# Kernel optimization log

Measured on AMD Instinct MI355X. Metric: run time of the kernel, lower is better.

## Reference

```python
import jax, jax.numpy as jnp
import numpy as np

B = 512       # batch
D = 256       # n_embd
NH = 4        # heads
NN = 8 * D // NH   # neurons per head = 512
NTOT = NH * NN     # 2048
DH = D // NH       # 64
K = 8              # thinking steps
EPS_LN = 1e-5


def _ln(x, g, b):
    mu = jnp.mean(x, axis=-1, keepdims=True)
    var = jnp.mean((x - mu) ** 2, axis=-1, keepdims=True)
    return (x - mu) * jax.lax.rsqrt(var + EPS_LN) * g + b


def setup_inputs() -> dict:
    key = jax.random.key(0)
    ks = jax.random.split(key, 12)
    s = 0.02
    w = lambda k, shape: (jax.random.normal(k, shape, jnp.float32) * s)
    return {
        "boards": jax.random.normal(ks[0], (B, 12, 8, 8), jnp.float32),
        # board_encoder: Linear(768,d) -> GELU -> LN(d) -> Linear(d,d); weights stored (in,out)
        "enc_w1": w(ks[1], (768, D)), "enc_b1": jnp.zeros((D,), jnp.float32),
        "enc_ln_g": jnp.ones((D,), jnp.float32), "enc_ln_b": jnp.zeros((D,), jnp.float32),
        "enc_w2": w(ks[2], (D, D)), "enc_b2": jnp.zeros((D,), jnp.float32),
        "xinit_w": w(ks[3], (D, NTOT)), "xinit_b": jnp.zeros((NTOT,), jnp.float32),
        "D_y": w(ks[4], (NH, D, NN)),
        "E": w(ks[5], (NTOT, D)),
        "D_x": w(ks[6], (NH, D, NN)),
        "By_w": w(ks[7], (D, D)),
        "Bx_w": w(ks[8], (D, D)),
        "lna_g": jnp.ones((D,), jnp.float32), "lna_b": jnp.zeros((D,), jnp.float32),
        "lnz_g": jnp.ones((D,), jnp.float32), "lnz_b": jnp.zeros((D,), jnp.float32),
        "log_damping": jnp.asarray(np.log(0.9 / 0.1), jnp.float32),
        "vh_w1": w(ks[9], (D, D // 2)), "vh_b1": jnp.zeros((D // 2,), jnp.float32),
        "vh_w2": w(ks[10], (D // 2, 1)), "vh_b2": jnp.zeros((1,), jnp.float32),
    }


def reference(boards, enc_w1, enc_b1, enc_ln_g, enc_ln_b, enc_w2, enc_b2,
              xinit_w, xinit_b, D_y, E, D_x, By_w, Bx_w,
              lna_g, lna_b, lnz_g, lnz_b, log_damping,
              vh_w1, vh_b1, vh_w2, vh_b2):
    Bn = boards.shape[0]
    flat = boards.reshape(Bn, 768)
    h = jax.nn.gelu(flat @ enc_w1 + enc_b1, approximate=False)
    h = _ln(h, enc_ln_g, enc_ln_b)
    b = h @ enc_w2 + enc_b2                      # (B, d)
    x0 = jax.nn.relu(b @ xinit_w + xinit_b)      # (B, n)
    rho0 = jnp.zeros((Bn, NH, NN, DH), boards.dtype)
    lam = jax.nn.sigmoid(log_damping)
    b_y = b @ By_w
    b_x = b @ Bx_w

    def step(carry, _):
        x, rho = carry
        x_h = x.reshape(Bn, NH, NN)
        a = jnp.einsum('bhnd,bhn->bhd', rho, x_h).reshape(Bn, D)   # read from scratchpad
        a_cond = _ln(a + b_y, lna_g, lna_b)
        g = jax.nn.relu(jnp.einsum('bd,hdn->bhn', a_cond, D_y))
        y = (g * x_h).reshape(Bn, NTOT)
        z = _ln(y @ E, lnz_g, lnz_b)
        dx = jax.nn.relu(jnp.einsum('bd,hdn->bhn', z + b_x, D_x))
        x_new = x + dx.reshape(Bn, NTOT)
        xh = x_new.reshape(Bn, NH, NN)
        x_write = xh / (jnp.linalg.norm(xh, axis=-1, keepdims=True) + 1e-8)
        z_h = z.reshape(Bn, NH, DH)
        rho_new = lam * rho + (1.0 - lam) * jnp.einsum('bhn,bhd->bhnd', x_write, z_h)
        return (x_new, rho_new), z

    (_, _), zs = jax.lax.scan(step, (x0, rho0), None, length=K)
    z_last = zs[-1]                              # (B, d) from final thinking step
    v = jnp.tanh(jax.nn.gelu(z_last @ vh_w1 + vh_b1, approximate=False) @ vh_w2 + vh_b2)
    return v                                     # (B, 1)
```

## Files before the change

kernel.cpp:

```cpp
#include <hip/hip_runtime.h>
#include <hip/hip_bf16.h>
#include <math.h>

#define B_ 512
#define D_ 256
#define NH_ 4
#define NN_ 512
#define NTOT_ 2048
#define DH_ 64
#define KSTEPS 8

typedef __attribute__((ext_vector_type(8))) short bf16x8;
typedef __attribute__((ext_vector_type(4))) float f32x4;

__device__ __forceinline__ float gelu_exact(float x) {
  return 0.5f * x * (1.0f + erff(x * 0.70710678118654752f));
}

__device__ __forceinline__ unsigned short f2b(float f) {
  union { float f; unsigned int u; } x; x.f = f;
  unsigned int u = x.u;
  unsigned int r = (u + 0x7FFFu + ((u >> 16) & 1u)) >> 16;
  return (unsigned short)r;
}

__device__ __forceinline__ float blockReduceSum256(float v, float* red) {
  int t = threadIdx.x;
  red[t] = v; __syncthreads();
  #pragma unroll
  for (int st = 128; st > 0; st >>= 1) {
    if (t < st) red[t] += red[t + st];
    __syncthreads();
  }
  float r = red[0];
  __syncthreads();
  return r;
}

template<int EPI>
__global__ __launch_bounds__(256) void gemm_mfma(
    const unsigned short* __restrict__ A, const unsigned short* __restrict__ W,
    const float* __restrict__ bias, const float* __restrict__ mul,
    const float* __restrict__ addto, float* __restrict__ outf,
    unsigned short* __restrict__ outb, int K, int N, int kchunk)
{
  __shared__ __align__(16) unsigned short As[64 * 64];
  __shared__ __align__(16) unsigned short Ws[64 * 64];
  const int t = threadIdx.x;
  const int lane = t & 63;
  const int w = t >> 6;
  const int wr = (w >> 1) * 32, wc = (w & 1) * 32;
  const int row0 = blockIdx.y * 64, col0 = blockIdx.x * 64;
  const int k0 = blockIdx.z * kchunk;

  f32x4 acc[2][2];
  #pragma unroll
  for (int i = 0; i < 2; i++)
    #pragma unroll
    for (int j = 0; j < 2; j++)
      acc[i][j] = (f32x4){0.f, 0.f, 0.f, 0.f};

  const int ar = t >> 3;
  const int ac = t & 7;

  for (int kt = 0; kt < kchunk; kt += 64) {
    const int kk = k0 + kt;
    #pragma unroll
    for (int p = 0; p < 2; p++) {
      int row = p * 32 + ar;
      int cs = ac ^ (row & 7);
      bf16x8 va = *(const bf16x8*)&A[(size_t)(row0 + row) * K + kk + cs * 8];
      *(bf16x8*)&As[row * 64 + ac * 8] = va;
      bf16x8 vb = *(const bf16x8*)&W[(size_t)(col0 + row) * K + kk + cs * 8];
      *(bf16x8*)&Ws[row * 64 + ac * 8] = vb;
    }
    __syncthreads();
    #pragma unroll
    for (int ks = 0; ks < 64; ks += 32) {
      bf16x8 af[2], bfr[2];
      #pragma unroll
      for (int i = 0; i < 2; i++) {
        int r = wr + i * 16 + (lane & 15);
        int cb = (ks + (lane >> 4) * 8) * 2;
        cb ^= (r & 7) << 4;
        af[i] = *(const bf16x8*)((const char*)As + r * 128 + cb);
      }
      #pragma unroll
      for (int j = 0; j < 2; j++) {
        int c = wc + j * 16 + (lane & 15);
        int cb = (ks + (lane >> 4) * 8) * 2;
        cb ^= (c & 7) << 4;
        bfr[j] = *(const bf16x8*)((const char*)Ws + c * 128 + cb);
      }
      #pragma unroll
      for (int i = 0; i < 2; i++)
        #pragma unroll
        for (int j = 0; j < 2; j++)
          acc[i][j] = __builtin_amdgcn_mfma_f32_16x16x32_bf16(af[i], bfr[j], acc[i][j], 0, 0, 0);
    }
    __syncthreads();
  }

  const int cr = (lane >> 4) * 4;
  const int cc = lane & 15;
  #pragma unroll
  for (int i = 0; i < 2; i++) {
    #pragma unroll
    for (int j = 0; j < 2; j++) {
      #pragma unroll
      for (int q = 0; q < 4; q++) {
        int r = row0 + wr + i * 16 + cr + q;
        int c = col0 + wc + j * 16 + cc;
        float v = acc[i][j][q];
        if (EPI == 0) {
          v += bias[c]; v = fmaxf(v, 0.f);
          outf[(size_t)r * N + c] = v;
        } else if (EPI == 1) {
          v = fmaxf(v, 0.f) * mul[(size_t)r * N + c];
          outb[(size_t)r * N + c] = f2b(v);
        } else if (EPI == 2) {
          outf[(size_t)blockIdx.z * (512 * (size_t)N) + (size_t)r * N + c] = v;
        } else {
          v = fmaxf(v, 0.f) + addto[(size_t)r * N + c];
          outf[(size_t)r * N + c] = v;
        }
      }
    }
  }
}

template<int ACT>
__global__ __launch_bounds__(256) void gemm_tile(
    const float* __restrict__ A, const float* __restrict__ W,
    const float* __restrict__ bias, float* __restrict__ out,
    int M, int N, int K, int kchunk)
{
  __shared__ float As[16][68];
  __shared__ float Bs[16][68];
  const int tid = threadIdx.x;
  const int row0 = blockIdx.y * 64;
  const int col0 = blockIdx.x * 64;
  const int k0 = blockIdx.z * kchunk;
  const int ty = tid >> 4, tx = tid & 15;
  const int ar = tid >> 4, ak = tid & 15;
  const int br = tid >> 6, bc = tid & 63;
  float acc[4][4] = {};
  for (int kk = k0; kk < k0 + kchunk; kk += 16) {
    #pragma unroll
    for (int i = 0; i < 4; i++) {
      int r = ar + i * 16;
      As[ak][r] = A[(size_t)(row0 + r) * K + kk + ak];
    }
    #pragma unroll
    for (int i = 0; i < 4; i++) {
      int kr = br + i * 4;
      Bs[kr][bc] = W[(size_t)(kk + kr) * N + col0 + bc];
    }
    __syncthreads();
    #pragma unroll
    for (int q = 0; q < 16; q++) {
      float4 av = *(const float4*)&As[q][ty * 4];
      float4 bv = *(const float4*)&Bs[q][tx * 4];
      float aa[4] = {av.x, av.y, av.z, av.w};
      float bb[4] = {bv.x, bv.y, bv.z, bv.w};
      #pragma unroll
      for (int i = 0; i < 4; i++)
        #pragma unroll
        for (int j = 0; j < 4; j++)
          acc[i][j] = fmaf(aa[i], bb[j], acc[i][j]);
    }
    __syncthreads();
  }
  const bool parts = (gridDim.z > 1);
  float* o = out + (parts ? (size_t)blockIdx.z * (size_t)M * N : (size_t)0);
  #pragma unroll
  for (int i = 0; i < 4; i++) {
    int r = row0 + ty * 4 + i;
    #pragma unroll
    for (int j = 0; j < 4; j++) {
      int c = col0 + tx * 4 + j;
      float v = acc[i][j];
      if (!parts) {
        if (bias) v += bias[c];
        if (ACT == 1) v = v > 0.f ? v : 0.f;
        else if (ACT == 2) v = gelu_exact(v);
      }
      o[(size_t)r * N + c] = v;
    }
  }
}

template<bool HEAD>
__global__ __launch_bounds__(256) void k_transpose_cvt(
    const float* __restrict__ in, unsigned short* __restrict__ out,
    int Kdim, int Ndim)
{
  __shared__ float T[64][65];
  const int n0 = blockIdx.x * 64, k0 = blockIdx.y * 64;
  const int tx = threadIdx.x & 63, ty = threadIdx.x >> 6;
  #pragma unroll
  for (int i = 0; i < 16; i++) {
    int k = k0 + ty + i * 4;
    int n = n0 + tx;
    float v;
    if (HEAD) v = in[((size_t)(n >> 9) * 256 + k) * 512 + (n & 511)];
    else      v = in[(size_t)k * Ndim + n];
    T[ty + i * 4][tx] = v;
  }
  __syncthreads();
  #pragma unroll
  for (int i = 0; i < 16; i++) {
    int n = n0 + ty + i * 4;
    out[(size_t)n * Kdim + k0 + tx] = f2b(T[tx][ty + i * 4]);
  }
}

__global__ __launch_bounds__(256) void k_cvt(
    const float* __restrict__ in, unsigned short* __restrict__ out, int n4)
{
  int i = blockIdx.x * 256 + threadIdx.x;
  if (i < n4) {
    float4 v = ((const float4*)in)[i];
    unsigned int u0 = (unsigned int)f2b(v.x) | ((unsigned int)f2b(v.y) << 16);
    unsigned int u1 = (unsigned int)f2b(v.z) | ((unsigned int)f2b(v.w) << 16);
    ((uint2*)out)[i] = make_uint2(u0, u1);
  }
}

__global__ __launch_bounds__(256) void k_ln_reduce(
    const float* __restrict__ in, int nparts, int stride,
    const float* __restrict__ pre_bias, int do_gelu,
    const float* __restrict__ g, const float* __restrict__ bta,
    const float* __restrict__ addvec, float* __restrict__ out,
    unsigned short* __restrict__ out2_bf)
{
  __shared__ float red[256];
  int b = blockIdx.x, d = threadIdx.x;
  float v = 0.f;
  for (int p = 0; p < nparts; p++) v += in[(size_t)p * stride + (size_t)b * 256 + d];
  if (pre_bias) v += pre_bias[d];
  if (do_gelu) v = gelu_exact(v);
  float mu = blockReduceSum256(v, red) * (1.f / 256.f);
  float c = v - mu;
  float var = blockReduceSum256(c * c, red) * (1.f / 256.f);
  float vn = c * rsqrtf(var + 1e-5f) * g[d] + bta[d];
  out[(size_t)b * 256 + d] = vn;
  if (out2_bf) out2_bf[(size_t)b * 256 + d] = f2b(vn + addvec[(size_t)b * 256 + d]);
}

__global__ __launch_bounds__(256) void step_a(
    const float* __restrict__ x, float* __restrict__ xw_hist,
    const float* __restrict__ z_hist, const float* __restrict__ b_y,
    const float* __restrict__ lna_g, const float* __restrict__ lna_b,
    const float* __restrict__ log_damp, int k, unsigned short* __restrict__ out)
{
  __shared__ float dots[KSTEPS][NH_];
  __shared__ float red[256];
  int b = blockIdx.x, t = threadIdx.x;
  int lane = t & 63, wv = t >> 6;
  float lam = 1.f / (1.f + expf(-log_damp[0]));
  const float* xb = x + (size_t)b * NTOT_;
  float xv[8];
  #pragma unroll
  for (int i = 0; i < 8; i++) xv[i] = xb[t * 8 + i];

  if (k >= 1) {
    float s = 0.f;
    #pragma unroll
    for (int i = 0; i < 8; i++) s += xv[i] * xv[i];
    #pragma unroll
    for (int m = 1; m < 64; m <<= 1) s += __shfl_xor(s, m, 64);
    float inv = 1.f / (sqrtf(s) + 1e-8f);
    float* xwout = xw_hist + ((size_t)(k - 1) * B_ + b) * NTOT_;
    #pragma unroll
    for (int i = 0; i < 8; i++) xwout[t * 8 + i] = xv[i] * inv;
    if (lane == 0) dots[k - 1][wv] = s * inv;
  }
  for (int j = 0; j < k - 1; j++) {
    const float* xwb = xw_hist + ((size_t)j * B_ + b) * NTOT_;
    float s = 0.f;
    #pragma unroll
    for (int i = 0; i < 8; i++) s += xv[i] * xwb[t * 8 + i];
    #pragma unroll
    for (int off = 32; off > 0; off >>= 1) s += __shfl_down(s, off, 64);
    if (lane == 0) dots[j][wv] = s;
  }
  __syncthreads();

  int d = t;
  float av = 0.f, lp = 1.f;
  for (int j = k - 1; j >= 0; j--) {
    av += (1.f - lam) * lp * dots[j][d >> 6] * z_hist[((size_t)j * B_ + b) * D_ + d];
    lp *= lam;
  }
  av += b_y[(size_t)b * D_ + d];
  float mu = blockReduceSum256(av, red) * (1.f / 256.f);
  float c = av - mu;
  float var = blockReduceSum256(c * c, red) * (1.f / 256.f);
  out[(size_t)b * D_ + d] = f2b(c * rsqrtf(var + 1e-5f) * lna_g[d] + lna_b[d]);
}

__global__ __launch_bounds__(128) void k_value2(
    const float* __restrict__ gbuf, const float* __restrict__ w2,
    const float* __restrict__ b2, float* __restrict__ out)
{
  int b = blockIdx.x * blockDim.x + threadIdx.x;
  float s = 0.f;
  #pragma unroll 8
  for (int i = 0; i < 128; i++) s += gbuf[(size_t)b * 128 + i] * w2[i];
  out[b] = tanhf(s + b2[0]);
}

extern "C" void kernel_launch(void* const* d_in, const int* in_sizes, int n_in,
                              void* d_out, int out_size, void* d_ws, size_t ws_size,
                              hipStream_t stream) {
  const float* boards   = (const float*)d_in[0];
  const float* enc_w1   = (const float*)d_in[1];
  const float* enc_b1   = (const float*)d_in[2];
  const float* enc_ln_g = (const float*)d_in[3];
  const float* enc_ln_b = (const float*)d_in[4];
  const float* enc_w2   = (const float*)d_in[5];
  const float* enc_b2   = (const float*)d_in[6];
  const float* xinit_w  = (const float*)d_in[7];
  const float* xinit_b  = (const float*)d_in[8];
  const float* D_y      = (const float*)d_in[9];
  const float* E        = (const float*)d_in[10];
  const float* D_x      = (const float*)d_in[11];
  const float* By_w     = (const float*)d_in[12];
  const float* Bx_w     = (const float*)d_in[13];
  const float* lna_g    = (const float*)d_in[14];
  const float* lna_b    = (const float*)d_in[15];
  const float* lnz_g    = (const float*)d_in[16];
  const float* lnz_b    = (const float*)d_in[17];
  const float* log_damp = (const float*)d_in[18];
  const float* vh_w1    = (const float*)d_in[19];
  const float* vh_b1    = (const float*)d_in[20];
  const float* vh_w2    = (const float*)d_in[21];
  const float* vh_b2    = (const float*)d_in[22];
  float* outp = (float*)d_out;

  float* ws = (float*)d_ws;
  size_t o = 0;
  float* x      = ws + o; o += (size_t)B_ * NTOT_;
  float* xw     = ws + o; o += (size_t)KSTEPS * B_ * NTOT_;
  float* zh     = ws + o; o += (size_t)KSTEPS * B_ * D_;
  float* hparts = ws + o; o += (size_t)3 * B_ * D_;
  float* h      = ws + o; o += (size_t)B_ * D_;
  float* bvec   = ws + o; o += (size_t)B_ * D_;
  float* b_y    = ws + o; o += (size_t)B_ * D_;
  float* b_x    = ws + o; o += (size_t)B_ * D_;
  float* zparts = ws + o; o += (size_t)8 * B_ * D_;
  float* gbuf   = ws + o; o += (size_t)B_ * 128;
  unsigned short* DyT     = (unsigned short*)(ws + o); o += (size_t)NTOT_ * D_ / 2;
  unsigned short* DxT     = (unsigned short*)(ws + o); o += (size_t)NTOT_ * D_ / 2;
  unsigned short* ET      = (unsigned short*)(ws + o); o += (size_t)D_ * NTOT_ / 2;
  unsigned short* xinitT  = (unsigned short*)(ws + o); o += (size_t)NTOT_ * D_ / 2;
  unsigned short* bvec_bf = (unsigned short*)(ws + o); o += (size_t)B_ * D_ / 2;
  unsigned short* acond_bf= (unsigned short*)(ws + o); o += (size_t)B_ * D_ / 2;
  unsigned short* zbx_bf  = (unsigned short*)(ws + o); o += (size_t)B_ * D_ / 2;
  unsigned short* y_bf    = (unsigned short*)(ws + o); o += (size_t)B_ * NTOT_ / 2;

  k_transpose_cvt<true ><<<dim3(32, 4), 256, 0, stream>>>(D_y,     DyT,    256, 2048);
  k_transpose_cvt<true ><<<dim3(32, 4), 256, 0, stream>>>(D_x,     DxT,    256, 2048);
  k_transpose_cvt<false><<<dim3(4, 32), 256, 0, stream>>>(E,       ET,     2048, 256);
  k_transpose_cvt<false><<<dim3(32, 4), 256, 0, stream>>>(xinit_w, xinitT, 256, 2048);

  gemm_tile<0><<<dim3(4, 8, 3), 256, 0, stream>>>(boards, enc_w1, nullptr, hparts,
                                                  B_, D_, 768, 256);
  k_ln_reduce<<<B_, 256, 0, stream>>>(hparts, 3, B_ * D_, enc_b1, 1,
                                      enc_ln_g, enc_ln_b, nullptr, h, nullptr);
  gemm_tile<0><<<dim3(4, 8, 1), 256, 0, stream>>>(h, enc_w2, enc_b2, bvec, B_, D_, D_, D_);
  k_cvt<<<dim3(B_ * D_ / 1024), 256, 0, stream>>>(bvec, bvec_bf, B_ * D_ / 4);
  gemm_tile<0><<<dim3(4, 8, 1), 256, 0, stream>>>(bvec, By_w, nullptr, b_y, B_, D_, D_, D_);
  gemm_tile<0><<<dim3(4, 8, 1), 256, 0, stream>>>(bvec, Bx_w, nullptr, b_x, B_, D_, D_, D_);
  gemm_mfma<0><<<dim3(32, 8, 1), 256, 0, stream>>>(bvec_bf, xinitT, xinit_b, nullptr,
                                                   nullptr, x, nullptr, 256, 2048, 256);

  for (int k = 0; k < KSTEPS; k++) {
    step_a<<<B_, 256, 0, stream>>>(x, xw, zh, b_y, lna_g, lna_b, log_damp, k, acond_bf);
    gemm_mfma<1><<<dim3(32, 8, 1), 256, 0, stream>>>(acond_bf, DyT, nullptr, x,
                                                     nullptr, nullptr, y_bf, 256, 2048, 256);
    gemm_mfma<2><<<dim3(4, 8, 8), 256, 0, stream>>>(y_bf, ET, nullptr, nullptr,
                                                    nullptr, zparts, nullptr, 2048, 256, 256);
    k_ln_reduce<<<B_, 256, 0, stream>>>(zparts, 8, B_ * D_, nullptr, 0, lnz_g, lnz_b,
                                        b_x, zh + (size_t)k * B_ * D_, zbx_bf);
    gemm_mfma<3><<<dim3(32, 8, 1), 256, 0, stream>>>(zbx_bf, DxT, nullptr, nullptr,
                                                     x, x, nullptr, 256, 2048, 256);
  }

  gemm_tile<2><<<dim3(2, 8, 1), 256, 0, stream>>>(zh + (size_t)(KSTEPS - 1) * B_ * D_,
                                                  vh_w1, vh_b1, gbuf, B_, 128, D_, D_);
  k_value2<<<4, 128, 0, stream>>>(gbuf, vh_w2, vh_b2, outp);
}
```

Measured before the change: 450.0 us.

## Double-buffer MFMA GEMM with direct global-to-LDS loads, smaller tiles, fewer launches

The bf16 MFMA GEMM now uses 64x32 tiles, so the grids double to 64x8 and 8x8x8 blocks. It double-buffers its LDS tiles and fills them with global_load_lds (direct global-to-LDS) when that builtin is available, so the next tile's load overlaps the current tile's MFMAs. The four weight transpose/convert kernels merge into one launch, the bvec bf16 conversion folds into the encoder GEMM epilogue, and the value head becomes a single fused kernel. The encoder's first GEMM is split into 8 K-chunks instead of 3 to raise parallelism. These changes aim to cut launch count and raise occupancy in the per-step GEMMs, at the cost of more redundant A-tile loads and a per-tile vmcnt(0) wait plus barrier.

New measurement: 413.7 us. -8.1%, faster.

```diff
diff --git a/kernel.cpp b/kernel.cpp
--- a/kernel.cpp
+++ b/kernel.cpp
@@ -13,6 +13,12 @@
 typedef __attribute__((ext_vector_type(8))) short bf16x8;
 typedef __attribute__((ext_vector_type(4))) float f32x4;
 
+#if __has_builtin(__builtin_amdgcn_global_load_lds)
+#define HAVE_GLL 1
+#else
+#define HAVE_GLL 0
+#endif
+
 __device__ __forceinline__ float gelu_exact(float x) {
   return 0.5f * x * (1.0f + erff(x * 0.70710678118654752f));
 }
@@ -36,6 +42,14 @@
   __syncthreads();
   return r;
 }
+
+#if HAVE_GLL
+__device__ __forceinline__ void load16_lds(const unsigned short* g, unsigned short* l) {
+  __builtin_amdgcn_global_load_lds(
+      (const __attribute__((address_space(1))) unsigned int*)g,
+      (__attribute__((address_space(3))) unsigned int*)l, 16, 0, 0);
+}
+#endif
 
 template<int EPI>
 __global__ __launch_bounds__(256) void gemm_mfma(
@@ -44,86 +58,110 @@
     const float* __restrict__ addto, float* __restrict__ outf,
     unsigned short* __restrict__ outb, int K, int N, int kchunk)
 {
-  __shared__ __align__(16) unsigned short As[64 * 64];
-  __shared__ __align__(16) unsigned short Ws[64 * 64];
+  __shared__ __align__(16) unsigned short As[2][64 * 64];
+  __shared__ __align__(16) unsigned short Ws[2][32 * 64];
   const int t = threadIdx.x;
   const int lane = t & 63;
   const int w = t >> 6;
-  const int wr = (w >> 1) * 32, wc = (w & 1) * 32;
-  const int row0 = blockIdx.y * 64, col0 = blockIdx.x * 64;
+  const int row0 = blockIdx.y * 64, col0 = blockIdx.x * 32;
   const int k0 = blockIdx.z * kchunk;
-
-  f32x4 acc[2][2];
-  #pragma unroll
-  for (int i = 0; i < 2; i++)
-    #pragma unroll
-    for (int j = 0; j < 2; j++)
-      acc[i][j] = (f32x4){0.f, 0.f, 0.f, 0.f};
-
-  const int ar = t >> 3;
-  const int ac = t & 7;
-
-  for (int kt = 0; kt < kchunk; kt += 64) {
-    const int kk = k0 + kt;
-    #pragma unroll
-    for (int p = 0; p < 2; p++) {
-      int row = p * 32 + ar;
-      int cs = ac ^ (row & 7);
-      bf16x8 va = *(const bf16x8*)&A[(size_t)(row0 + row) * K + kk + cs * 8];
-      *(bf16x8*)&As[row * 64 + ac * 8] = va;
-      bf16x8 vb = *(const bf16x8*)&W[(size_t)(col0 + row) * K + kk + cs * 8];
-      *(bf16x8*)&Ws[row * 64 + ac * 8] = vb;
-    }
-    __syncthreads();
-    #pragma unroll
-    for (int ks = 0; ks < 64; ks += 32) {
-      bf16x8 af[2], bfr[2];
-      #pragma unroll
-      for (int i = 0; i < 2; i++) {
-        int r = wr + i * 16 + (lane & 15);
-        int cb = (ks + (lane >> 4) * 8) * 2;
-        cb ^= (r & 7) << 4;
-        af[i] = *(const bf16x8*)((const char*)As + r * 128 + cb);
-      }
+  const int nt = kchunk >> 6;
+  const int lr = lane & 15, lk = lane >> 4;
+  const int l3 = lane >> 3, cch = lane & 7;
+
+  f32x4 acc[2];
+  acc[0] = (f32x4){0.f, 0.f, 0.f, 0.f};
+  acc[1] = (f32x4){0.f, 0.f, 0.f, 0.f};
+
+#if HAVE_GLL
+  #define STAGE(tt)                                                              \
+    {                                                                            \
+      int buf_ = (tt) & 1;                                                       \
+      int kk_ = k0 + (tt) * 64;                                                  \
+      _Pragma("unroll")                                                          \
+      for (int p = 0; p < 2; p++) {                                              \
+        int r_ = (w * 2 + p) * 8 + l3;                                           \
+        load16_lds(&A[(size_t)(row0 + r_) * K + kk_ + ((cch ^ (r_ & 7)) << 3)],  \
+                   &As[buf_][(w * 2 + p) * 512]);                                \
+      }                                                                          \
+      int rw_ = w * 8 + l3;                                                      \
+      load16_lds(&W[(size_t)(col0 + rw_) * K + kk_ + ((cch ^ (rw_ & 7)) << 3)],  \
+                 &Ws[buf_][w * 512]);                                            \
+    }
+
+  STAGE(0);
+  for (int tt = 0; tt < nt; tt++) {
+    asm volatile("s_waitcnt vmcnt(0)" ::: "memory");
+    __builtin_amdgcn_s_barrier();
+    asm volatile("" ::: "memory");
+    if (tt + 1 < nt) STAGE(tt + 1);
+    const unsigned short* Ab = As[tt & 1];
+    const unsigned short* Wb = Ws[tt & 1];
+    #pragma unroll
+    for (int ks = 0; ks < 2; ks++) {
+      int q = ks * 4 + lk;
+      int r = w * 16 + lr;
+      bf16x8 af = *(const bf16x8*)&Ab[r * 64 + ((q ^ (r & 7)) << 3)];
       #pragma unroll
       for (int j = 0; j < 2; j++) {
-        int c = wc + j * 16 + (lane & 15);
-        int cb = (ks + (lane >> 4) * 8) * 2;
-        cb ^= (c & 7) << 4;
-        bfr[j] = *(const bf16x8*)((const char*)Ws + c * 128 + cb);
+        int c = j * 16 + lr;
+        bf16x8 bf = *(const bf16x8*)&Wb[c * 64 + ((q ^ (c & 7)) << 3)];
+        acc[j] = __builtin_amdgcn_mfma_f32_16x16x32_bf16(af, bf, acc[j], 0, 0, 0);
       }
+    }
+  }
+  #undef STAGE
+#else
+  for (int tt = 0; tt < nt; tt++) {
+    int buf_ = tt & 1;
+    int kk_ = k0 + tt * 64;
+    #pragma unroll
+    for (int p = 0; p < 2; p++) {
+      int r_ = (w * 2 + p) * 8 + l3;
+      bf16x8 v = *(const bf16x8*)&A[(size_t)(row0 + r_) * K + kk_ + ((cch ^ (r_ & 7)) << 3)];
+      *(bf16x8*)&As[buf_][r_ * 64 + (cch << 3)] = v;
+    }
+    int rw_ = w * 8 + l3;
+    bf16x8 vw = *(const bf16x8*)&W[(size_t)(col0 + rw_) * K + kk_ + ((cch ^ (rw_ & 7)) << 3)];
+    *(bf16x8*)&Ws[buf_][rw_ * 64 + (cch << 3)] = vw;
+    __syncthreads();
+    const unsigned short* Ab = As[buf_];
+    const unsigned short* Wb = Ws[buf_];
+    #pragma unroll
+    for (int ks = 0; ks < 2; ks++) {
+      int q = ks * 4 + lk;
+      int r = w * 16 + lr;
+      bf16x8 af = *(const bf16x8*)&Ab[r * 64 + ((q ^ (r & 7)) << 3)];
       #pragma unroll
-      for (int i = 0; i < 2; i++)
-        #pragma unroll
-        for (int j = 0; j < 2; j++)
-          acc[i][j] = __builtin_amdgcn_mfma_f32_16x16x32_bf16(af[i], bfr[j], acc[i][j], 0, 0, 0);
-    }
-    __syncthreads();
-  }
-
-  const int cr = (lane >> 4) * 4;
-  const int cc = lane & 15;
-  #pragma unroll
-  for (int i = 0; i < 2; i++) {
-    #pragma unroll
-    for (int j = 0; j < 2; j++) {
-      #pragma unroll
-      for (int q = 0; q < 4; q++) {
-        int r = row0 + wr + i * 16 + cr + q;
-        int c = col0 + wc + j * 16 + cc;
-        float v = acc[i][j][q];
-        if (EPI == 0) {
-          v += bias[c]; v = fmaxf(v, 0.f);
-          outf[(size_t)r * N + c] = v;
-        } else if (EPI == 1) {
-          v = fmaxf(v, 0.f) * mul[(size_t)r * N + c];
-          outb[(size_t)r * N + c] = f2b(v);
-        } else if (EPI == 2) {
-          outf[(size_t)blockIdx.z * (512 * (size_t)N) + (size_t)r * N + c] = v;
-        } else {
-          v = fmaxf(v, 0.f) + addto[(size_t)r * N + c];
-          outf[(size_t)r * N + c] = v;
-        }
+      for (int j = 0; j < 2; j++) {
+        int c = j * 16 + lr;
+        bf16x8 bf = *(const bf16x8*)&Wb[c * 64 + ((q ^ (c & 7)) << 3)];
+        acc[j] = __builtin_amdgcn_mfma_f32_16x16x32_bf16(af, bf, acc[j], 0, 0, 0);
+      }
+    }
+    __syncthreads();
+  }
+#endif
+
+  const int cr = lk * 4;
+  #pragma unroll
+  for (int j = 0; j < 2; j++) {
+    #pragma unroll
+    for (int q = 0; q < 4; q++) {
+      int r = row0 + w * 16 + cr + q;
+      int c = col0 + j * 16 + lr;
+      float v = acc[j][q];
+      if (EPI == 0) {
+        v += bias[c]; v = fmaxf(v, 0.f);
+        outf[(size_t)r * N + c] = v;
+      } else if (EPI == 1) {
+        v = fmaxf(v, 0.f) * mul[(size_t)r * N + c];
+        outb[(size_t)r * N + c] = f2b(v);
+      } else if (EPI == 2) {
+        outf[(size_t)blockIdx.z * ((size_t)512 * N) + (size_t)r * N + c] = v;
+      } else {
+        v = fmaxf(v, 0.f) + addto[(size_t)r * N + c];
+        outf[(size_t)r * N + c] = v;
       }
     }
   }
@@ -133,7 +171,7 @@
 __global__ __launch_bounds__(256) void gemm_tile(
     const float* __restrict__ A, const float* __restrict__ W,
     const float* __restrict__ bias, float* __restrict__ out,
-    int M, int N, int K, int kchunk)
+    unsigned short* __restrict__ outb, int M, int N, int K, int kchunk)
 {
   __shared__ float As[16][68];
   __shared__ float Bs[16][68];
@@ -182,48 +220,44 @@
       float v = acc[i][j];
       if (!parts) {
         if (bias) v += bias[c];
-        if (ACT == 1) v = v > 0.f ? v : 0.f;
-        else if (ACT == 2) v = gelu_exact(v);
+        if (ACT == 2) v = gelu_exact(v);
       }
       o[(size_t)r * N + c] = v;
-    }
-  }
-}
-
-template<bool HEAD>
-__global__ __launch_bounds__(256) void k_transpose_cvt(
-    const float* __restrict__ in, unsigned short* __restrict__ out,
-    int Kdim, int Ndim)
+      if (!parts && outb) outb[(size_t)r * N + c] = f2b(v);
+    }
+  }
+}
+
+__global__ __launch_bounds__(256) void k_prep(
+    const float* __restrict__ D_y, const float* __restrict__ D_x,
+    const float* __restrict__ xinit_w, const float* __restrict__ E,
+    unsigned short* __restrict__ DyT, unsigned short* __restrict__ DxT,
+    unsigned short* __restrict__ xinitT, unsigned short* __restrict__ ET)
 {
   __shared__ float T[64][65];
-  const int n0 = blockIdx.x * 64, k0 = blockIdx.y * 64;
+  const float* in; unsigned short* out; int Kd, Nd, head, nx;
+  switch (blockIdx.y) {
+    case 0:  in = D_y;     out = DyT;    Kd = 256;  Nd = 2048; head = 1; nx = 32; break;
+    case 1:  in = D_x;     out = DxT;    Kd = 256;  Nd = 2048; head = 1; nx = 32; break;
+    case 2:  in = xinit_w; out = xinitT; Kd = 256;  Nd = 2048; head = 0; nx = 32; break;
+    default: in = E;       out = ET;     Kd = 2048; Nd = 256;  head = 0; nx = 4;  break;
+  }
+  const int n0 = (blockIdx.x % nx) * 64, k0 = (blockIdx.x / nx) * 64;
   const int tx = threadIdx.x & 63, ty = threadIdx.x >> 6;
   #pragma unroll
   for (int i = 0; i < 16; i++) {
     int k = k0 + ty + i * 4;
     int n = n0 + tx;
     float v;
-    if (HEAD) v = in[((size_t)(n >> 9) * 256 + k) * 512 + (n & 511)];
-    else      v = in[(size_t)k * Ndim + n];
+    if (head) v = in[((size_t)(n >> 9) * 256 + k) * 512 + (n & 511)];
+    else      v = in[(size_t)k * Nd + n];
     T[ty + i * 4][tx] = v;
   }
   __syncthreads();
   #pragma unroll
   for (int i = 0; i < 16; i++) {
     int n = n0 + ty + i * 4;
-    out[(size_t)n * Kdim + k0 + tx] = f2b(T[tx][ty + i * 4]);
-  }
-}
-
-__global__ __launch_bounds__(256) void k_cvt(
-    const float* __restrict__ in, unsigned short* __restrict__ out, int n4)
-{
-  int i = blockIdx.x * 256 + threadIdx.x;
-  if (i < n4) {
-    float4 v = ((const float4*)in)[i];
-    unsigned int u0 = (unsigned int)f2b(v.x) | ((unsigned int)f2b(v.y) << 16);
-    unsigned int u1 = (unsigned int)f2b(v.z) | ((unsigned int)f2b(v.w) << 16);
-    ((uint2*)out)[i] = make_uint2(u0, u1);
+    out[(size_t)n * Kd + k0 + tx] = f2b(T[tx][ty + i * 4]);
   }
 }
 
@@ -300,15 +334,25 @@
   out[(size_t)b * D_ + d] = f2b(c * rsqrtf(var + 1e-5f) * lna_g[d] + lna_b[d]);
 }
 
-__global__ __launch_bounds__(128) void k_value2(
-    const float* __restrict__ gbuf, const float* __restrict__ w2,
+__global__ __launch_bounds__(128) void k_value(
+    const float* __restrict__ z, const float* __restrict__ w1,
+    const float* __restrict__ b1, const float* __restrict__ w2,
     const float* __restrict__ b2, float* __restrict__ out)
 {
-  int b = blockIdx.x * blockDim.x + threadIdx.x;
+  __shared__ float red[128];
+  int b = blockIdx.x, j = threadIdx.x;
+  const float* zr = z + (size_t)b * 256;
   float s = 0.f;
   #pragma unroll 8
-  for (int i = 0; i < 128; i++) s += gbuf[(size_t)b * 128 + i] * w2[i];
-  out[b] = tanhf(s + b2[0]);
+  for (int i = 0; i < 256; i++) s += zr[i] * w1[(size_t)i * 128 + j];
+  float g = gelu_exact(s + b1[j]) * w2[j];
+  red[j] = g; __syncthreads();
+  #pragma unroll
+  for (int st = 64; st > 0; st >>= 1) {
+    if (j < st) red[j] += red[j + st];
+    __syncthreads();
+  }
+  if (j == 0) out[b] = tanhf(red[0] + b2[0]);
 }
 
 extern "C" void kernel_launch(void* const* d_in, const int* in_sizes, int n_in,
@@ -344,13 +388,12 @@
   float* x      = ws + o; o += (size_t)B_ * NTOT_;
   float* xw     = ws + o; o += (size_t)KSTEPS * B_ * NTOT_;
   float* zh     = ws + o; o += (size_t)KSTEPS * B_ * D_;
-  float* hparts = ws + o; o += (size_t)3 * B_ * D_;
+  float* hparts = ws + o; o += (size_t)8 * B_ * D_;
   float* h      = ws + o; o += (size_t)B_ * D_;
   float* bvec   = ws + o; o += (size_t)B_ * D_;
   float* b_y    = ws + o; o += (size_t)B_ * D_;
   float* b_x    = ws + o; o += (size_t)B_ * D_;
   float* zparts = ws + o; o += (size_t)8 * B_ * D_;
-  float* gbuf   = ws + o; o += (size_t)B_ * 128;
   unsigned short* DyT     = (unsigned short*)(ws + o); o += (size_t)NTOT_ * D_ / 2;
   unsigned short* DxT     = (unsigned short*)(ws + o); o += (size_t)NTOT_ * D_ / 2;
   unsigned short* ET      = (unsigned short*)(ws + o); o += (size_t)D_ * NTOT_ / 2;
@@ -360,35 +403,33 @@
   unsigned short* zbx_bf  = (unsigned short*)(ws + o); o += (size_t)B_ * D_ / 2;
   unsigned short* y_bf    = (unsigned short*)(ws + o); o += (size_t)B_ * NTOT_ / 2;
 
-  k_transpose_cvt<true ><<<dim3(32, 4), 256, 0, stream>>>(D_y,     DyT,    256, 2048);
-  k_transpose_cvt<true ><<<dim3(32, 4), 256, 0, stream>>>(D_x,     DxT,    256, 2048);
-  k_transpose_cvt<false><<<dim3(4, 32), 256, 0, stream>>>(E,       ET,     2048, 256);
-  k_transpose_cvt<false><<<dim3(32, 4), 256, 0, stream>>>(xinit_w, xinitT, 256, 2048);
-
-  gemm_tile<0><<<dim3(4, 8, 3), 256, 0, stream>>>(boards, enc_w1, nullptr, hparts,
-                                                  B_, D_, 768, 256);
-  k_ln_reduce<<<B_, 256, 0, stream>>>(hparts, 3, B_ * D_, enc_b1, 1,
+  k_prep<<<dim3(128, 4), 256, 0, stream>>>(D_y, D_x, xinit_w, E, DyT, DxT, xinitT, ET);
+
+  gemm_tile<0><<<dim3(4, 8, 8), 256, 0, stream>>>(boards, enc_w1, nullptr, hparts,
+                                                  nullptr, B_, D_, 768, 96);
+  k_ln_reduce<<<B_, 256, 0, stream>>>(hparts, 8, B_ * D_, enc_b1, 1,
                                       enc_ln_g, enc_ln_b, nullptr, h, nullptr);
-  gemm_tile<0><<<dim3(4, 8, 1), 256, 0, stream>>>(h, enc_w2, enc_b2, bvec, B_, D_, D_, D_);
-  k_cvt<<<dim3(B_ * D_ / 1024), 256, 0, stream>>>(bvec, bvec_bf, B_ * D_ / 4);
-  gemm_tile<0><<<dim3(4, 8, 1), 256, 0, stream>>>(bvec, By_w, nullptr, b_y, B_, D_, D_, D_);
-  gemm_tile<0><<<dim3(4, 8, 1), 256, 0, stream>>>(bvec, Bx_w, nullptr, b_x, B_, D_, D_, D_);
-  gemm_mfma<0><<<dim3(32, 8, 1), 256, 0, stream>>>(bvec_bf, xinitT, xinit_b, nullptr,
+  gemm_tile<0><<<dim3(4, 8, 1), 256, 0, stream>>>(h, enc_w2, enc_b2, bvec, bvec_bf,
+                                                  B_, D_, D_, D_);
+  gemm_tile<0><<<dim3(4, 8, 1), 256, 0, stream>>>(bvec, By_w, nullptr, b_y, nullptr,
+                                                  B_, D_, D_, D_);
+  gemm_tile<0><<<dim3(4, 8, 1), 256, 0, stream>>>(bvec, Bx_w, nullptr, b_x, nullptr,
+                                                  B_, D_, D_, D_);
+  gemm_mfma<0><<<dim3(64, 8, 1), 256, 0, stream>>>(bvec_bf, xinitT, xinit_b, nullptr,
                                                    nullptr, x, nullptr, 256, 2048, 256);
 
   for (int k = 0; k < KSTEPS; k++) {
     step_a<<<B_, 256, 0, stream>>>(x, xw, zh, b_y, lna_g, lna_b, log_damp, k, acond_bf);
-    gemm_mfma<1><<<dim3(32, 8, 1), 256, 0, stream>>>(acond_bf, DyT, nullptr, x,
+    gemm_mfma<1><<<dim3(64, 8, 1), 256, 0, stream>>>(acond_bf, DyT, nullptr, x,
                                                      nullptr, nullptr, y_bf, 256, 2048, 256);
-    gemm_mfma<2><<<dim3(4, 8, 8), 256, 0, stream>>>(y_bf, ET, nullptr, nullptr,
+    gemm_mfma<2><<<dim3(8, 8, 8), 256, 0, stream>>>(y_bf, ET, nullptr, nullptr,
                                                     nullptr, zparts, nullptr, 2048, 256, 256);
     k_ln_reduce<<<B_, 256, 0, stream>>>(zparts, 8, B_ * D_, nullptr, 0, lnz_g, lnz_b,
                                         b_x, zh + (size_t)k * B_ * D_, zbx_bf);
-    gemm_mfma<3><<<dim3(32, 8, 1), 256, 0, stream>>>(zbx_bf, DxT, nullptr, nullptr,
+    gemm_mfma<3><<<dim3(64, 8, 1), 256, 0, stream>>>(zbx_bf, DxT, nullptr, nullptr,
                                                      x, x, nullptr, 256, 2048, 256);
   }
 
-  gemm_tile<2><<<dim3(2, 8, 1), 256, 0, stream>>>(zh + (size_t)(KSTEPS - 1) * B_ * D_,
-                                                  vh_w1, vh_b1, gbuf, B_, 128, D_, D_);
-  k_value2<<<4, 128, 0, stream>>>(gbuf, vh_w2, vh_b2, outp);
-}
+  k_value<<<B_, 128, 0, stream>>>(zh + (size_t)(KSTEPS - 1) * B_ * D_,
+                                  vh_w1, vh_b1, vh_w2, vh_b2, outp);
+}
```
